# Optimization experiments

Measured on AMD Instinct MI355X. Metric: run time of the kernel, lower is better.

Reference implementation:

```python
import jax, jax.numpy as jnp
import numpy as np

B, D_IN, UNITS = 8192, 4096, 4096

def setup_inputs() -> dict:
    key = jax.random.key(0)
    k1, k2 = jax.random.split(key)
    x = jax.random.normal(k1, (B, D_IN), dtype=jnp.float32)
    kernel = jax.random.normal(k2, (D_IN, UNITS), dtype=jnp.float32) * 0.02  # glorot-ish scale
    bias = jnp.zeros((UNITS,), dtype=jnp.float32)
    return {"x": x, "kernel": kernel, "bias": bias}

def reference(x, kernel, bias):
    # BinaryDense: binarize weights via sign, then dense matmul + bias
    kernel_bin = jnp.sign(kernel)                     # [D_IN, UNITS], values in {-1,0,+1}
    out = jnp.matmul(x, kernel_bin) + bias            # [B, UNITS]
    return out
```

## Files before the change

### kernel.cpp

```cpp
#include <hip/hip_runtime.h>
#include <stdint.h>


typedef int int4v __attribute__((ext_vector_type(4)));

constexpr int M = 8192, N = 4096, K = 4096;
constexpr int BM = 128, BN = 128, BK = 64;

__device__ __forceinline__ void gload_lds16(const void* g, void* l) {
  __builtin_amdgcn_global_load_lds(
      (const __attribute__((address_space(1))) unsigned int*)g,
      (__attribute__((address_space(3))) unsigned int*)l, 16, 0, 0);
}

__global__ __launch_bounds__(256) void quant_x_kernel(const float* __restrict__ x,
                                                      signed char* __restrict__ xq,
                                                      float* __restrict__ rscale) {
  const int row = blockIdx.x;
  const int t = threadIdx.x;
  const float* xr = x + (size_t)row * K;
  float4 v[4];
  float mx = 0.f;
#pragma unroll
  for (int i = 0; i < 4; ++i) {
    v[i] = *(const float4*)(xr + t * 16 + i * 4);
    mx = fmaxf(mx, fmaxf(fmaxf(fabsf(v[i].x), fabsf(v[i].y)),
                         fmaxf(fabsf(v[i].z), fabsf(v[i].w))));
  }
#pragma unroll
  for (int off = 32; off >= 1; off >>= 1)
    mx = fmaxf(mx, __shfl_xor(mx, off, 64));
  __shared__ float smax[4];
  if ((t & 63) == 0) smax[t >> 6] = mx;
  __syncthreads();
  const float rm = fmaxf(fmaxf(smax[0], smax[1]), fmaxf(smax[2], smax[3]));
  const float s = (rm > 0.f) ? 127.f / rm : 0.f;
  if (t == 0) rscale[row] = (rm > 0.f) ? rm / 127.f : 0.f;
  uint32_t o[4];
#pragma unroll
  for (int i = 0; i < 4; ++i) {
    float f[4] = {v[i].x, v[i].y, v[i].z, v[i].w};
    uint32_t p = 0;
#pragma unroll
    for (int j = 0; j < 4; ++j) {
      int q = (int)rintf(f[j] * s);
      p |= ((uint32_t)(uint8_t)(signed char)q) << (8 * j);
    }
    o[i] = p;
  }
  *(int4v*)(xq + (size_t)row * K + t * 16) = (int4v){(int)o[0], (int)o[1], (int)o[2], (int)o[3]};
}

__global__ __launch_bounds__(256) void sign_t_kernel(const float* __restrict__ w,
                                                     signed char* __restrict__ wq) {
  __shared__ __align__(16) signed char tile[64 * 68];
  const int n0 = blockIdx.x * 64, k0 = blockIdx.y * 64;
  const int t = threadIdx.x;
#pragma unroll
  for (int i = 0; i < 4; ++i) {
    int kl = (t >> 4) + i * 16;
    int nl = (t & 15) * 4;
    float4 v = *(const float4*)(w + (size_t)(k0 + kl) * N + n0 + nl);
    uint32_t p = 0;
    p |= ((uint32_t)(uint8_t)(signed char)((v.x > 0.f) - (v.x < 0.f)));
    p |= ((uint32_t)(uint8_t)(signed char)((v.y > 0.f) - (v.y < 0.f))) << 8;
    p |= ((uint32_t)(uint8_t)(signed char)((v.z > 0.f) - (v.z < 0.f))) << 16;
    p |= ((uint32_t)(uint8_t)(signed char)((v.w > 0.f) - (v.w < 0.f))) << 24;
    *(uint32_t*)(tile + kl * 68 + nl) = p;
  }
  __syncthreads();
  const int nl = t >> 2;
  const int kc = (t & 3) * 16;
  uint32_t o[4] = {0, 0, 0, 0};
#pragma unroll
  for (int j = 0; j < 16; ++j)
    o[j >> 2] |= ((uint32_t)(uint8_t)tile[(kc + j) * 68 + nl]) << (8 * (j & 3));
  *(int4v*)(wq + (size_t)(n0 + nl) * K + k0 + kc) =
      (int4v){(int)o[0], (int)o[1], (int)o[2], (int)o[3]};
}

__global__ __launch_bounds__(256) void gemm_bin_kernel(
    const signed char* __restrict__ Xq,
    const signed char* __restrict__ Wq,
    const float* __restrict__ rscale,
    const float* __restrict__ bias,
    float* __restrict__ out) {
  __shared__ __align__(16) signed char Alds[BM * BK];
  __shared__ __align__(16) signed char Blds[BN * BK];

  const int tid = threadIdx.x;
  const int w = tid >> 6;
  const int lane = tid & 63;
  const int wm = w & 1, wn = w >> 1;
  const int m0 = blockIdx.y * BM;
  const int n0 = blockIdx.x * BN;
  const int quad = lane >> 4;
  const int l16 = lane & 15;

  int4v acc[4][4];
#pragma unroll
  for (int i = 0; i < 4; ++i)
#pragma unroll
    for (int j = 0; j < 4; ++j)
      acc[i][j] = (int4v){0, 0, 0, 0};

  for (int k0 = 0; k0 < K; k0 += BK) {
#pragma unroll
    for (int it = 0; it < 2; ++it) {
      int p = it * 256 + tid;
      int row = p >> 2;
      int chunk = (p & 3) ^ ((row >> 1) & 3);
      gload_lds16(Xq + (size_t)(m0 + row) * K + k0 + chunk * 16,
                  Alds + (size_t)(it * 256 + w * 64) * 16);
    }
#pragma unroll
    for (int it = 0; it < 2; ++it) {
      int p = it * 256 + tid;
      int row = p >> 2;
      int chunk = (p & 3) ^ ((row >> 1) & 3);
      gload_lds16(Wq + (size_t)(n0 + row) * K + k0 + chunk * 16,
                  Blds + (size_t)(it * 256 + w * 64) * 16);
    }
    __syncthreads();

    int4v a[4], b[4];
#pragma unroll
    for (int mi = 0; mi < 4; ++mi) {
      int r = wm * 64 + mi * 16 + l16;
      int cpos = (r << 2) | (quad ^ ((r >> 1) & 3));
      a[mi] = *(const int4v*)(Alds + (size_t)cpos * 16);
    }
#pragma unroll
    for (int ni = 0; ni < 4; ++ni) {
      int r = wn * 64 + ni * 16 + l16;
      int cpos = (r << 2) | (quad ^ ((r >> 1) & 3));
      b[ni] = *(const int4v*)(Blds + (size_t)cpos * 16);
    }
#pragma unroll
    for (int mi = 0; mi < 4; ++mi)
#pragma unroll
      for (int ni = 0; ni < 4; ++ni)
        acc[mi][ni] = __builtin_amdgcn_mfma_i32_16x16x64_i8(a[mi], b[ni], acc[mi][ni], 0, 0, 0);

    __syncthreads();
  }

  float sc[4][4];
#pragma unroll
  for (int mi = 0; mi < 4; ++mi) {
    int rbase = m0 + wm * 64 + mi * 16 + quad * 4;
#pragma unroll
    for (int r = 0; r < 4; ++r) sc[mi][r] = rscale[rbase + r];
  }
#pragma unroll
  for (int ni = 0; ni < 4; ++ni) {
    int col = n0 + wn * 64 + ni * 16 + l16;
    float bv = bias[col];
#pragma unroll
    for (int mi = 0; mi < 4; ++mi) {
      int rbase = m0 + wm * 64 + mi * 16 + quad * 4;
#pragma unroll
      for (int r = 0; r < 4; ++r)
        out[(size_t)(rbase + r) * N + col] = (float)acc[mi][ni][r] * sc[mi][r] + bv;
    }
  }
}

extern "C" void kernel_launch(void* const* d_in, const int* in_sizes, int n_in,
                              void* d_out, int out_size, void* d_ws, size_t ws_size,
                              hipStream_t stream) {
  const float* x = (const float*)d_in[0];
  const float* kern = (const float*)d_in[1];
  const float* bias = (const float*)d_in[2];
  float* out = (float*)d_out;

  signed char* Xq = (signed char*)d_ws;
  signed char* Wq = Xq + (size_t)M * K;
  float* rscale = (float*)(Wq + (size_t)N * K);

  quant_x_kernel<<<M, 256, 0, stream>>>(x, Xq, rscale);
  sign_t_kernel<<<dim3(N / 64, K / 64), dim3(256), 0, stream>>>(kern, Wq);
  gemm_bin_kernel<<<dim3(N / BN, M / BM), 256, 0, stream>>>(Xq, Wq, rscale, bias, out);
}
```

Measured before the change: 428.7 us.

## Rewrite int8 GEMM with 256x256 double-buffered tiles and fuse prep kernels

Merges the x-quantization and weight sign-transpose kernels into a single launch that branches on block index. Replaces the GEMM with a 512-thread, 256x256x128 tiled kernel that uses 32x32x32 int8 MFMA, a double-buffered 128KB LDS with an XOR swizzle, and software-pipelined LDS register reads interleaved with MFMA, plus s_setprio hints. The goal is more data reuse per byte loaded and overlap of global-to-LDS copies with compute, so the GEMM runs closer to peak MFMA throughput. In exchange the kernel uses much more LDS and registers, which limits occupancy, and the synchronisation is more intricate.

```diff
diff --git a/kernel.cpp b/kernel.cpp
--- a/kernel.cpp
+++ b/kernel.cpp
@@ -3,9 +3,11 @@
 
 
 typedef int int4v __attribute__((ext_vector_type(4)));
+typedef int int16v __attribute__((ext_vector_type(16)));
 
 constexpr int M = 8192, N = 4096, K = 4096;
-constexpr int BM = 128, BN = 128, BK = 64;
+constexpr int BM = 256, BN = 256, BK = 128;
+constexpr int NT = K / BK;
 
 __device__ __forceinline__ void gload_lds16(const void* g, void* l) {
   __builtin_amdgcn_global_load_lds(
@@ -13,155 +15,197 @@
       (__attribute__((address_space(3))) unsigned int*)l, 16, 0, 0);
 }
 
-__global__ __launch_bounds__(256) void quant_x_kernel(const float* __restrict__ x,
-                                                      signed char* __restrict__ xq,
-                                                      float* __restrict__ rscale) {
-  const int row = blockIdx.x;
+#define FENCE asm volatile("" ::: "memory")
+
+__global__ __launch_bounds__(256) void prep_kernel(const float* __restrict__ x,
+                                                   signed char* __restrict__ xq,
+                                                   float* __restrict__ rscale,
+                                                   const float* __restrict__ w,
+                                                   signed char* __restrict__ wq) {
   const int t = threadIdx.x;
-  const float* xr = x + (size_t)row * K;
-  float4 v[4];
-  float mx = 0.f;
-#pragma unroll
-  for (int i = 0; i < 4; ++i) {
-    v[i] = *(const float4*)(xr + t * 16 + i * 4);
-    mx = fmaxf(mx, fmaxf(fmaxf(fabsf(v[i].x), fabsf(v[i].y)),
-                         fmaxf(fabsf(v[i].z), fabsf(v[i].w))));
-  }
-#pragma unroll
-  for (int off = 32; off >= 1; off >>= 1)
-    mx = fmaxf(mx, __shfl_xor(mx, off, 64));
-  __shared__ float smax[4];
-  if ((t & 63) == 0) smax[t >> 6] = mx;
-  __syncthreads();
-  const float rm = fmaxf(fmaxf(smax[0], smax[1]), fmaxf(smax[2], smax[3]));
-  const float s = (rm > 0.f) ? 127.f / rm : 0.f;
-  if (t == 0) rscale[row] = (rm > 0.f) ? rm / 127.f : 0.f;
-  uint32_t o[4];
-#pragma unroll
-  for (int i = 0; i < 4; ++i) {
-    float f[4] = {v[i].x, v[i].y, v[i].z, v[i].w};
-    uint32_t p = 0;
-#pragma unroll
-    for (int j = 0; j < 4; ++j) {
-      int q = (int)rintf(f[j] * s);
-      p |= ((uint32_t)(uint8_t)(signed char)q) << (8 * j);
-    }
-    o[i] = p;
-  }
-  *(int4v*)(xq + (size_t)row * K + t * 16) = (int4v){(int)o[0], (int)o[1], (int)o[2], (int)o[3]};
-}
-
-__global__ __launch_bounds__(256) void sign_t_kernel(const float* __restrict__ w,
-                                                     signed char* __restrict__ wq) {
-  __shared__ __align__(16) signed char tile[64 * 68];
-  const int n0 = blockIdx.x * 64, k0 = blockIdx.y * 64;
-  const int t = threadIdx.x;
-#pragma unroll
-  for (int i = 0; i < 4; ++i) {
-    int kl = (t >> 4) + i * 16;
-    int nl = (t & 15) * 4;
-    float4 v = *(const float4*)(w + (size_t)(k0 + kl) * N + n0 + nl);
-    uint32_t p = 0;
-    p |= ((uint32_t)(uint8_t)(signed char)((v.x > 0.f) - (v.x < 0.f)));
-    p |= ((uint32_t)(uint8_t)(signed char)((v.y > 0.f) - (v.y < 0.f))) << 8;
-    p |= ((uint32_t)(uint8_t)(signed char)((v.z > 0.f) - (v.z < 0.f))) << 16;
-    p |= ((uint32_t)(uint8_t)(signed char)((v.w > 0.f) - (v.w < 0.f))) << 24;
-    *(uint32_t*)(tile + kl * 68 + nl) = p;
-  }
-  __syncthreads();
-  const int nl = t >> 2;
-  const int kc = (t & 3) * 16;
-  uint32_t o[4] = {0, 0, 0, 0};
-#pragma unroll
-  for (int j = 0; j < 16; ++j)
-    o[j >> 2] |= ((uint32_t)(uint8_t)tile[(kc + j) * 68 + nl]) << (8 * (j & 3));
-  *(int4v*)(wq + (size_t)(n0 + nl) * K + k0 + kc) =
-      (int4v){(int)o[0], (int)o[1], (int)o[2], (int)o[3]};
-}
-
-__global__ __launch_bounds__(256) void gemm_bin_kernel(
+  if (blockIdx.x < M) {
+    const int row = blockIdx.x;
+    const float* xr = x + (size_t)row * K;
+    float4 v[4];
+    float mx = 0.f;
+#pragma unroll
+    for (int i = 0; i < 4; ++i) {
+      v[i] = *(const float4*)(xr + t * 16 + i * 4);
+      mx = fmaxf(mx, fmaxf(fmaxf(fabsf(v[i].x), fabsf(v[i].y)),
+                           fmaxf(fabsf(v[i].z), fabsf(v[i].w))));
+    }
+#pragma unroll
+    for (int off = 32; off >= 1; off >>= 1)
+      mx = fmaxf(mx, __shfl_xor(mx, off, 64));
+    __shared__ float smax[4];
+    if ((t & 63) == 0) smax[t >> 6] = mx;
+    __syncthreads();
+    const float rm = fmaxf(fmaxf(smax[0], smax[1]), fmaxf(smax[2], smax[3]));
+    const float s = (rm > 0.f) ? 127.f / rm : 0.f;
+    if (t == 0) rscale[row] = (rm > 0.f) ? rm / 127.f : 0.f;
+    uint32_t o[4];
+#pragma unroll
+    for (int i = 0; i < 4; ++i) {
+      float f[4] = {v[i].x, v[i].y, v[i].z, v[i].w};
+      uint32_t p = 0;
+#pragma unroll
+      for (int j = 0; j < 4; ++j) {
+        int q = (int)rintf(f[j] * s);
+        p |= ((uint32_t)(uint8_t)(signed char)q) << (8 * j);
+      }
+      o[i] = p;
+    }
+    *(int4v*)(xq + (size_t)row * K + t * 16) =
+        (int4v){(int)o[0], (int)o[1], (int)o[2], (int)o[3]};
+  } else {
+    __shared__ __align__(16) signed char tile[64 * 68];
+    const int idx = blockIdx.x - M;
+    const int n0 = (idx & 63) * 64, k0 = (idx >> 6) * 64;
+#pragma unroll
+    for (int i = 0; i < 4; ++i) {
+      int kl = (t >> 4) + i * 16;
+      int nl = (t & 15) * 4;
+      float4 v = *(const float4*)(w + (size_t)(k0 + kl) * N + n0 + nl);
+      uint32_t p = 0;
+      p |= ((uint32_t)(uint8_t)(signed char)((v.x > 0.f) - (v.x < 0.f)));
+      p |= ((uint32_t)(uint8_t)(signed char)((v.y > 0.f) - (v.y < 0.f))) << 8;
+      p |= ((uint32_t)(uint8_t)(signed char)((v.z > 0.f) - (v.z < 0.f))) << 16;
+      p |= ((uint32_t)(uint8_t)(signed char)((v.w > 0.f) - (v.w < 0.f))) << 24;
+      *(uint32_t*)(tile + kl * 68 + nl) = p;
+    }
+    __syncthreads();
+    const int nl = t >> 2;
+    const int kc = (t & 3) * 16;
+    uint32_t o[4] = {0, 0, 0, 0};
+#pragma unroll
+    for (int j = 0; j < 16; ++j)
+      o[j >> 2] |= ((uint32_t)(uint8_t)tile[(kc + j) * 68 + nl]) << (8 * (j & 3));
+    *(int4v*)(wq + (size_t)(n0 + nl) * K + k0 + kc) =
+        (int4v){(int)o[0], (int)o[1], (int)o[2], (int)o[3]};
+  }
+}
+
+
+#define RD_SET(AN, BN_, P, KK)                                                    \
+  {                                                                               \
+    _Pragma("unroll") for (int mi_ = 0; mi_ < 4; ++mi_) {                         \
+      const int r_ = wm * 128 + mi_ * 32 + l31;                                   \
+      AN[mi_] = *(const int4v*)(smem + (P)*65536 + r_ * 128 +                     \
+                                ((((KK)*2 + hi) ^ (r_ & 7)) * 16));               \
+    }                                                                             \
+    _Pragma("unroll") for (int ni_ = 0; ni_ < 2; ++ni_) {                         \
+      const int r_ = wn * 64 + ni_ * 32 + l31;                                    \
+      BN_[ni_] = *(const int4v*)(smem + (P)*65536 + 32768 + r_ * 128 +            \
+                                 ((((KK)*2 + hi) ^ (r_ & 7)) * 16));              \
+    }                                                                             \
+  }
+
+#define MM(AN, BN_)                                                               \
+  {                                                                               \
+    __builtin_amdgcn_s_setprio(1);                                                \
+    _Pragma("unroll") for (int mi_ = 0; mi_ < 4; ++mi_) {                         \
+      _Pragma("unroll") for (int ni_ = 0; ni_ < 2; ++ni_) {                       \
+        acc[mi_][ni_] = __builtin_amdgcn_mfma_i32_32x32x32_i8(                    \
+            AN[mi_], BN_[ni_], acc[mi_][ni_], 0, 0, 0);                           \
+      }                                                                           \
+    }                                                                             \
+    __builtin_amdgcn_s_setprio(0);                                                \
+  }
+
+#define TILE(P, NP, TS, MORE)                                                     \
+  {                                                                               \
+    RD_SET(aY, bY, P, 1);                                                         \
+    if (MORE) stage(NP, TS);                                                      \
+    MM(aX, bX);                                                           \
+    RD_SET(aX, bX, P, 2);                                                         \
+    MM(aY, bY);                                                           \
+    RD_SET(aY, bY, P, 3);                                                         \
+    MM(aX, bX);                                                           \
+    asm volatile("s_waitcnt vmcnt(0)" ::: "memory");                              \
+    __builtin_amdgcn_s_barrier();                                                 \
+    FENCE;                                                                        \
+    if (MORE) RD_SET(aX, bX, NP, 0);                                              \
+    MM(aY, bY);                                                           \
+    FENCE;                                                                        \
+    __builtin_amdgcn_s_barrier();                                                 \
+    FENCE;                                                                        \
+  }
+
+__global__ __launch_bounds__(512, 2) void gemm_bin_kernel(
     const signed char* __restrict__ Xq,
     const signed char* __restrict__ Wq,
     const float* __restrict__ rscale,
     const float* __restrict__ bias,
     float* __restrict__ out) {
-  __shared__ __align__(16) signed char Alds[BM * BK];
-  __shared__ __align__(16) signed char Blds[BN * BK];
+  __shared__ __align__(16) signed char smem[131072];
 
   const int tid = threadIdx.x;
   const int w = tid >> 6;
   const int lane = tid & 63;
-  const int wm = w & 1, wn = w >> 1;
-  const int m0 = blockIdx.y * BM;
-  const int n0 = blockIdx.x * BN;
-  const int quad = lane >> 4;
-  const int l16 = lane & 15;
-
-  int4v acc[4][4];
+  const int wm = w >> 2;
+  const int wn = w & 3;
+  const int hi = lane >> 5;
+  const int l31 = lane & 31;
+  const size_t m0 = (size_t)blockIdx.y * BM;
+  const size_t n0 = (size_t)blockIdx.x * BN;
+
+  int16v acc[4][2];
 #pragma unroll
   for (int i = 0; i < 4; ++i)
 #pragma unroll
-    for (int j = 0; j < 4; ++j)
-      acc[i][j] = (int4v){0, 0, 0, 0};
-
-  for (int k0 = 0; k0 < K; k0 += BK) {
-#pragma unroll
-    for (int it = 0; it < 2; ++it) {
-      int p = it * 256 + tid;
-      int row = p >> 2;
-      int chunk = (p & 3) ^ ((row >> 1) & 3);
-      gload_lds16(Xq + (size_t)(m0 + row) * K + k0 + chunk * 16,
-                  Alds + (size_t)(it * 256 + w * 64) * 16);
-    }
-#pragma unroll
-    for (int it = 0; it < 2; ++it) {
-      int p = it * 256 + tid;
-      int row = p >> 2;
-      int chunk = (p & 3) ^ ((row >> 1) & 3);
-      gload_lds16(Wq + (size_t)(n0 + row) * K + k0 + chunk * 16,
-                  Blds + (size_t)(it * 256 + w * 64) * 16);
-    }
-    __syncthreads();
-
-    int4v a[4], b[4];
-#pragma unroll
-    for (int mi = 0; mi < 4; ++mi) {
-      int r = wm * 64 + mi * 16 + l16;
-      int cpos = (r << 2) | (quad ^ ((r >> 1) & 3));
-      a[mi] = *(const int4v*)(Alds + (size_t)cpos * 16);
-    }
-#pragma unroll
-    for (int ni = 0; ni < 4; ++ni) {
-      int r = wn * 64 + ni * 16 + l16;
-      int cpos = (r << 2) | (quad ^ ((r >> 1) & 3));
-      b[ni] = *(const int4v*)(Blds + (size_t)cpos * 16);
-    }
-#pragma unroll
-    for (int mi = 0; mi < 4; ++mi)
-#pragma unroll
-      for (int ni = 0; ni < 4; ++ni)
-        acc[mi][ni] = __builtin_amdgcn_mfma_i32_16x16x64_i8(a[mi], b[ni], acc[mi][ni], 0, 0, 0);
-
-    __syncthreads();
-  }
-
-  float sc[4][4];
+    for (int j = 0; j < 2; ++j)
+#pragma unroll
+      for (int r = 0; r < 16; ++r) acc[i][j][r] = 0;
+  int4v aX[4], bX[2], aY[4], bY[2];
+
+  auto stage = [&](int pb, int t) {
+    signed char* lb = smem + pb * 65536;
+#pragma unroll
+    for (int it = 0; it < 4; ++it) {
+      int pos = it * 512 + tid;
+      int row = pos >> 3, s = pos & 7;
+      int qg = s ^ (row & 7);
+      gload_lds16(Xq + (m0 + row) * (size_t)K + (size_t)t * BK + qg * 16,
+                  lb + row * 128 + s * 16);
+    }
+#pragma unroll
+    for (int it = 0; it < 4; ++it) {
+      int pos = it * 512 + tid;
+      int row = pos >> 3, s = pos & 7;
+      int qg = s ^ (row & 7);
+      gload_lds16(Wq + (n0 + row) * (size_t)K + (size_t)t * BK + qg * 16,
+                  lb + 32768 + row * 128 + s * 16);
+    }
+  };
+
+  stage(0, 0);
+  asm volatile("s_waitcnt vmcnt(0)" ::: "memory");
+  __builtin_amdgcn_s_barrier();
+  FENCE;
+  RD_SET(aX, bX, 0, 0);
+
+#pragma unroll 1
+  for (int tt = 0; tt < NT; tt += 2) {
+    TILE(0, 1, tt + 1, true)
+    TILE(1, 0, tt + 2, (tt + 2 < NT))
+  }
+
 #pragma unroll
   for (int mi = 0; mi < 4; ++mi) {
-    int rbase = m0 + wm * 64 + mi * 16 + quad * 4;
-#pragma unroll
-    for (int r = 0; r < 4; ++r) sc[mi][r] = rscale[rbase + r];
-  }
-#pragma unroll
-  for (int ni = 0; ni < 4; ++ni) {
-    int col = n0 + wn * 64 + ni * 16 + l16;
-    float bv = bias[col];
-#pragma unroll
-    for (int mi = 0; mi < 4; ++mi) {
-      int rbase = m0 + wm * 64 + mi * 16 + quad * 4;
-#pragma unroll
-      for (int r = 0; r < 4; ++r)
-        out[(size_t)(rbase + r) * N + col] = (float)acc[mi][ni][r] * sc[mi][r] + bv;
+    const size_t rbase = m0 + wm * 128 + mi * 32;
+    float sc[4][4];
+#pragma unroll
+    for (int q = 0; q < 4; ++q)
+      *(float4*)sc[q] = *(const float4*)(rscale + rbase + hi * 4 + q * 8);
+#pragma unroll
+    for (int ni = 0; ni < 2; ++ni) {
+      const size_t col = n0 + wn * 64 + ni * 32 + l31;
+      const float bv = bias[col];
+#pragma unroll
+      for (int r = 0; r < 16; ++r) {
+        const int row = (r & 3) + 8 * (r >> 2) + 4 * hi;
+        out[(rbase + row) * N + col] = (float)acc[mi][ni][r] * sc[r >> 2][r & 3] + bv;
+      }
     }
   }
 }
@@ -178,7 +222,6 @@
   signed char* Wq = Xq + (size_t)M * K;
   float* rscale = (float*)(Wq + (size_t)N * K);
 
-  quant_x_kernel<<<M, 256, 0, stream>>>(x, Xq, rscale);
-  sign_t_kernel<<<dim3(N / 64, K / 64), dim3(256), 0, stream>>>(kern, Wq);
-  gemm_bin_kernel<<<dim3(N / BN, M / BM), 256, 0, stream>>>(Xq, Wq, rscale, bias, out);
-}
+  prep_kernel<<<M + (N / 64) * (K / 64), 256, 0, stream>>>(x, Xq, rscale, kern, Wq);
+  gemm_bin_kernel<<<dim3(N / BN, M / BM), 512, 0, stream>>>(Xq, Wq, rscale, bias, out);
+}
```

After: 391.0 us. 1.1x faster.
